# Optimization experiments

Hardware: AMD Instinct MI355X
Metric: run time of the kernel (lower is better)

Reference implementation:

```python
import jax, jax.numpy as jnp
import numpy as np

N, M, C = 32768, 8192, 128
K = 3            # number of interpolation neighbors (PointNet++/RepSurf FP)
EPS_BN = 1e-5    # torch BatchNorm1d default eps
EPS_D = 1e-8     # RepSurf dist_recip eps


def setup_inputs() -> dict:
    key = jax.random.key(0)
    ks = jax.random.split(key, 16)
    s = 0.05
    inp = {
        "pos1": jax.random.normal(ks[0], (N, 3), jnp.float32),
        "pos2": jax.random.normal(ks[1], (M, 3), jnp.float32),
        "feat2": jax.random.normal(ks[2], (M, C), jnp.float32),
    }
    # MLP stack [128,128,128]: Linear + BatchNorm1d (gamma/beta) per layer
    for i in range(3):
        inp[f"W{i}"] = jax.random.normal(ks[3 + i], (C, C), jnp.float32) * s
        inp[f"b{i}"] = jnp.zeros((C,), jnp.float32)
        inp[f"g{i}"] = jnp.ones((C,), jnp.float32)
        inp[f"be{i}"] = jnp.zeros((C,), jnp.float32)
    return inp


def _lin_bn_relu(x, W, b, g, be):
    # Linear -> BatchNorm1d (training-mode batch stats, biased var) -> ReLU
    y = x @ W.T + b
    m = y.mean(axis=0)
    v = y.var(axis=0)
    return jax.nn.relu((y - m) * jax.lax.rsqrt(v + EPS_BN) * g + be)


def reference(pos1, pos2, feat2, W0, b0, g0, be0, W1, b1, g1, be1, W2, b2, g2, be2):
    # squared pairwise distances [N, M] (memory-bound: 1 GB fp32)
    d = ((pos1 ** 2).sum(-1, keepdims=True)
         + (pos2 ** 2).sum(-1)[None, :]
         - 2.0 * (pos1 @ pos2.T))
    neg_d, idx = jax.lax.top_k(-d, K)          # 3 nearest neighbors
    dk = jnp.maximum(-neg_d, 0.0)              # [N, K] squared dists
    w = 1.0 / (dk + EPS_D)
    w = w / w.sum(-1, keepdims=True)           # inverse-distance weights
    # gather neighbor features and interpolate: [N, K, C] -> [N, C]
    interp = jnp.einsum('nkc,nk->nc', feat2[idx], w)
    x = _lin_bn_relu(interp, W0, b0, g0, be0)
    x = _lin_bn_relu(x, W1, b1, g1, be1)
    x = _lin_bn_relu(x, W2, b2, g2, be2)
    return x
```

## Files before the change

### kernel.cpp

```cpp
#include <hip/hip_runtime.h>
#include <hip/hip_fp16.h>
#include <math.h>

#define NQ 32768
#define MC 8192
#define CC 128
#define EPS_BN 1e-5f
#define EPS_D  1e-8

#define DBL_BIG 1e300
#define IDX_BIG 0x7fffffff

#define QB  64
#define TB  256
#define PCE 2048
#define NT  32
#define KM7 0xFFFFFF80u
#define KMASK 0xFFFFE000u
#define IMASK 0x1FFFu
#define NSURV 48
#define KNN_B ((NQ / QB) * 4)
#define GEMM_B (NQ / 64)
#define NGRP 8

typedef __attribute__((ext_vector_type(8))) short bf16x8;
typedef __attribute__((ext_vector_type(8))) _Float16 half8;
typedef __attribute__((ext_vector_type(4))) float floatx4;
typedef __attribute__((ext_vector_type(16))) float floatx16;
typedef unsigned short ushort_t;

__device__ __forceinline__ unsigned bf16pair(float a, float b) {
    unsigned ua = __float_as_uint(a); ua = (ua + 0x7FFFu + ((ua >> 16) & 1u)) >> 16;
    unsigned ub = __float_as_uint(b); ub = (ub + 0x7FFFu + ((ub >> 16) & 1u)) >> 16;
    return ua | (ub << 16);
}
__device__ __forceinline__ ushort_t bf16one(float a) {
    unsigned ua = __float_as_uint(a);
    return (ushort_t)((ua + 0x7FFFu + ((ua >> 16) & 1u)) >> 16);
}
__device__ __forceinline__ float bflo(unsigned u) { return __uint_as_float(u << 16); }
__device__ __forceinline__ float bfhi(unsigned u) { return __uint_as_float(u & 0xFFFF0000u); }

__device__ __forceinline__ void ins3(float& k0, float& k1, float& k2, float x) {
    const float n0 = fminf(k0, x);
    const float n1 = __builtin_amdgcn_fmed3f(k0, k1, x);
    const float n2 = __builtin_amdgcn_fmed3f(k1, k2, x);
    k0 = n0; k1 = n1; k2 = n2;
}

__device__ __forceinline__ unsigned vandor(unsigned d, unsigned m, unsigned ir) {
    unsigned r;
    asm("v_and_or_b32 %0, %1, %2, %3" : "=v"(r) : "v"(d), "s"(m), "v"(ir));
    return r;
}

#define PK2(a, b) ((unsigned)__half_as_ushort(a) | ((unsigned)__half_as_ushort(b) << 16))

__global__ __launch_bounds__(TB) void pack_kernel(const float* __restrict__ pos2,
                                                  uint4* __restrict__ ptile,
                                                  float4* __restrict__ pos2f4) {
    const int c = blockIdx.x * TB + threadIdx.x;
    const float x = pos2[c * 3 + 0];
    const float y = pos2[c * 3 + 1];
    const float z = pos2[c * 3 + 2];
    float4 p4; p4.x = x; p4.y = y; p4.z = z; p4.w = 0.f;
    pos2f4[c] = p4;
    const __half chx = __float2half(x); const float fchx = __half2float(chx);
    const __half chy = __float2half(y); const float fchy = __half2float(chy);
    const __half chz = __float2half(z); const float fchz = __half2float(chz);
    const __half clx = __float2half(x - fchx);
    const __half cly = __float2half(y - fchy);
    const __half clz = __float2half(z - fchz);
    const double X = (double)fchx + (double)__half2float(clx);
    const double Y = (double)fchy + (double)__half2float(cly);
    const double Z = (double)fchz + (double)__half2float(clz);
    const double hc = 0.5 * (X * X + Y * Y + Z * Z);
// ... 94 lines not shown
    float c0 = KINIT, c1 = KINIT, c2 = KINIT;
    float e0 = KINIT, e1 = KINIT, e2 = KINIT;
    unsigned i0 = 0u, i1 = 1u, i2 = 2u, i3 = 3u;
    const unsigned km7 = KM7;
    const floatx16 zc = {0.f,0.f,0.f,0.f,0.f,0.f,0.f,0.f,0.f,0.f,0.f,0.f,0.f,0.f,0.f,0.f};

#define KEY1(v, ir, K0, K1, K2) { \
        const unsigned u_ = vandor(__float_as_uint(v), km7, ir); \
        ins3(K0, K1, K2, __uint_as_float(u_)); }
#define KEYS(d) { \
        KEY1(d[0],  i0, a0, a1, a2); KEY1(d[1],  i1, a0, a1, a2); \
        KEY1(d[2],  i2, a0, a1, a2); KEY1(d[3],  i3, a0, a1, a2); \
        KEY1(d[4],  i0, b0, b1, b2); KEY1(d[5],  i1, b0, b1, b2); \
        KEY1(d[6],  i2, b0, b1, b2); KEY1(d[7],  i3, b0, b1, b2); \
        KEY1(d[8],  i0, c0, c1, c2); KEY1(d[9],  i1, c0, c1, c2); \
        KEY1(d[10], i2, c0, c1, c2); KEY1(d[11], i3, c0, c1, c2); \
        KEY1(d[12], i0, e0, e1, e2); KEY1(d[13], i1, e0, e1, e2); \
        KEY1(d[14], i2, e0, e1, e2); KEY1(d[15], i3, e0, e1, e2); \
        i0 += 4u; i1 += 4u; i2 += 4u; i3 += 4u; }

    uint4 LA = LD(0);
    uint4 LB = LD(1);
    for (int t = 0; t < NT; t += 2) {
        const floatx16 dv = __builtin_amdgcn_mfma_f32_32x32x16_f16(*(const half8*)&LA, bqh, zc, 0, 0, 0);
        LA = LD(t + 2);
        KEYS(dv);
        const floatx16 dw = __builtin_amdgcn_mfma_f32_32x32x16_f16(*(const half8*)&LB, bqh, zc, 0, 0, 0);
        LB = LD(t + 3);
        KEYS(dw);
    }
#undef LD
#undef KEYS
#undef KEY1

#define REKEY(kf, q) __uint_as_float((__float_as_uint(kf) & KMASK) | \
        (unsigned)(cw + (int)((__float_as_uint(kf) & 0x7Fu) >> 2) * 32 + \
                   (int)(__float_as_uint(kf) & 3u) + 8 * (q) + 4 * h))
    float m0 = KINIT, m1 = KINIT, m2 = KINIT;
    ins3(m0, m1, m2, REKEY(a0, 0)); ins3(m0, m1, m2, REKEY(a1, 0)); ins3(m0, m1, m2, REKEY(a2, 0));
    ins3(m0, m1, m2, REKEY(b0, 1)); ins3(m0, m1, m2, REKEY(b1, 1)); ins3(m0, m1, m2, REKEY(b2, 1));
    ins3(m0, m1, m2, REKEY(c0, 2)); ins3(m0, m1, m2, REKEY(c1, 2)); ins3(m0, m1, m2, REKEY(c2, 2));
    ins3(m0, m1, m2, REKEY(e0, 3)); ins3(m0, m1, m2, REKEY(e1, 3)); ins3(m0, m1, m2, REKEY(e2, 3));
#undef REKEY

    {
        const int q = bq * QB + qt * 32 + col;
        unsigned* dst = skeys + (size_t)q * NSURV + piece * 12 + wh * 6 + h * 3;
        dst[0] = __float_as_uint(m0);
        dst[1] = __float_as_uint(m1);
        dst[2] = __float_as_uint(m2);
    }
}

template <int MODE>
__global__ __launch_bounds__(256) void gemm_mfma(const void* __restrict__ Xsrc_,
                                                 const unsigned* __restrict__ skeys,
                                                 const float* __restrict__ pos1,
                                                 const float4* __restrict__ pos2f4,
                                                 const float* __restrict__ statsIn,
                                                 const float* __restrict__ gIn,
                                                 const float* __restrict__ beIn,
                                                 const ushort_t* __restrict__ Wb,
                                                 const float* __restrict__ bias,
                                                 ushort_t* __restrict__ Y,
                                                 float* __restrict__ statsOut) {
    __shared__ __align__(16) short xa[64][136];
    __shared__ __align__(16) short wb[128][136];
    __shared__ float blk_s[CC], blk_q[CC];
    __shared__ float sc_l[CC], sh_l[CC];

    const int row0 = blockIdx.x * 64;

    if constexpr (MODE == 0) {
        const float* feat2 = (const float*)Xsrc_;
        __shared__ int   lidx[QB][3];
        __shared__ float lw[QB][3];
        {
            double* rrd = (double*)&xa[0][0];
            int*    rri = (int*)&wb[0][0];
            const int ql = threadIdx.x >> 2;
            const int pp = threadIdx.x & 3;
            const int qg = row0 + ql;
            const double qx = (double)pos1[qg * 3 + 0];
            const double qy = (double)pos1[qg * 3 + 1];
            const double qz = (double)pos1[qg * 3 + 2];
            double b0 = DBL_BIG, b1 = DBL_BIG, b2 = DBL_BIG;
            int    j0 = IDX_BIG, j1 = IDX_BIG, j2 = IDX_BIG;
            const uint4* kp = (const uint4*)(skeys + (size_t)qg * NSURV + pp * 12);
#pragma unroll
            for (int gi = 0; gi < 3; ++gi) {
                const uint4 kk = kp[gi];
                const unsigned ks[4] = {kk.x, kk.y, kk.z, kk.w};
#pragma unroll
                for (int u = 0; u < 4; ++u) {
                    const int id = (int)(ks[u] & IMASK);
                    const float4 cf = pos2f4[id];
                    const double x = (double)cf.x;
                    const double y = (double)cf.y;
                    const double z = (double)cf.z;
                    const double ax = qx - x, ay = qy - y, az = qz - z;
                    const double d = ax * ax + ay * ay + az * az;
                    const bool l2 = (d < b2) || (d == b2 && id < j2);
                    if (l2) {
                        const bool l1 = (d < b1) || (d == b1 && id < j1);
                        const bool l0 = (d < b0) || (d == b0 && id < j0);
                        b2 = l1 ? b1 : d;              j2 = l1 ? j1 : id;
                        b1 = l1 ? (l0 ? b0 : d) : b1;  j1 = l1 ? (l0 ? j0 : id) : j1;
                        b0 = l0 ? d : b0;              j0 = l0 ? id : j0;
                    }
                }
            }
            const int base = (ql * 4 + pp) * 3;
            rrd[base + 0] = b0; rri[base + 0] = j0;
            rrd[base + 1] = b1; rri[base + 1] = j1;
            rrd[base + 2] = b2; rri[base + 2] = j2;
            __syncthreads();
            if (threadIdx.x < QB) {
                const int qq = threadIdx.x;
                double c0 = DBL_BIG, c1 = DBL_BIG, c2 = DBL_BIG;
                int    i0 = IDX_BIG, i1 = IDX_BIG, i2 = IDX_BIG;
#pragma unroll
                for (int s = 0; s < 12; ++s) {
                    const double d = rrd[qq * 12 + s];
                    const int   id = rri[qq * 12 + s];
                    const bool l2 = (d < c2) || (d == c2 && id < i2);
                    if (l2) {
                        const bool l1 = (d < c1) || (d == c1 && id < i1);
                        const bool l0 = (d < c0) || (d == c0 && id < i0);
                        c2 = l1 ? c1 : d;              i2 = l1 ? i1 : id;
                        c1 = l1 ? (l0 ? c0 : d) : c1;  i1 = l1 ? (l0 ? i0 : id) : i1;
                        c0 = l0 ? d : c0;              i0 = l0 ? id : i0;
                    }
                }
                const double r0 = 1.0 / (c0 + EPS_D);
                const double r1 = 1.0 / (c1 + EPS_D);
                const double r2 = 1.0 / (c2 + EPS_D);
                const double inv = 1.0 / (r0 + r1 + r2);
                lidx[qq][0] = i0; lidx[qq][1] = i1; lidx[qq][2] = i2;
                lw[qq][0] = (float)(r0 * inv);
                lw[qq][1] = (float)(r1 * inv);
                lw[qq][2] = (float)(r2 * inv);
            }
            __syncthreads();
        }
        if (threadIdx.x < CC) { blk_s[threadIdx.x] = 0.f; blk_q[threadIdx.x] = 0.f; }
#pragma unroll
        for (int e = threadIdx.x; e < 64 * 32; e += 256) {
            const int r = e >> 5, c4 = e & 31;
            const int i0 = lidx[r][0], i1 = lidx[r][1], i2 = lidx[r][2];
            const float w0 = lw[r][0], w1 = lw[r][1], w2 = lw[r][2];
            const float4 f0 = *(const float4*)&feat2[(size_t)i0 * CC + c4 * 4];
            const float4 f1 = *(const float4*)&feat2[(size_t)i1 * CC + c4 * 4];
            const float4 f2 = *(const float4*)&feat2[(size_t)i2 * CC + c4 * 4];
            float4 v;
            v.x = w0 * f0.x + w1 * f1.x + w2 * f2.x;
            v.y = w0 * f0.y + w1 * f1.y + w2 * f2.y;
            v.z = w0 * f0.z + w1 * f1.z + w2 * f2.z;
            v.w = w0 * f0.w + w1 * f1.w + w2 * f2.w;
            unsigned* dst = (unsigned*)&xa[r][0];
            dst[c4 * 2 + 0] = bf16pair(v.x, v.y);
            dst[c4 * 2 + 1] = bf16pair(v.z, v.w);
        }
    } else {
        const ushort_t* Xbf = (const ushort_t*)Xsrc_;
        if (threadIdx.x < CC) {
            const int c = threadIdx.x;
            float s = 0.f, q = 0.f;
#pragma unroll
            for (int gr = 0; gr < NGRP; ++gr) {
                s += statsIn[gr * 256 + c];
                q += statsIn[gr * 256 + CC + c];
            }
            const float m = s * (1.f / (float)NQ);
            const float v = fmaf(-m, m, q * (1.f / (float)NQ));
            const float rstd = rsqrtf(v + EPS_BN);
            const float scl = gIn[c] * rstd;
            sc_l[c] = scl;
            sh_l[c] = fmaf(-m, scl, beIn[c]);
            blk_s[c] = 0.f; blk_q[c] = 0.f;
        }
        __syncthreads();
#pragma unroll
        for (int e = threadIdx.x; e < 64 * 16; e += 256) {
            const int r = e >> 4, c8 = e & 15;
            const uint4 u = *(const uint4*)&Xbf[(size_t)(row0 + r) * CC + c8 * 8];
            const float4 s0 = *(const float4*)&sc_l[c8 * 8];
            const float4 s1 = *(const float4*)&sc_l[c8 * 8 + 4];
            const float4 h0 = *(const float4*)&sh_l[c8 * 8];
            const float4 h1 = *(const float4*)&sh_l[c8 * 8 + 4];
            const float v0 = fmaxf(fmaf(bflo(u.x), s0.x, h0.x), 0.f);
            const float v1 = fmaxf(fmaf(bfhi(u.x), s0.y, h0.y), 0.f);
            const float v2 = fmaxf(fmaf(bflo(u.y), s0.z, h0.z), 0.f);
            const float v3 = fmaxf(fmaf(bfhi(u.y), s0.w, h0.w), 0.f);
            const float v4 = fmaxf(fmaf(bflo(u.z), s1.x, h1.x), 0.f);
            const float v5 = fmaxf(fmaf(bfhi(u.z), s1.y, h1.y), 0.f);
            const float v6 = fmaxf(fmaf(bflo(u.w), s1.z, h1.z), 0.f);
            const float v7 = fmaxf(fmaf(bfhi(u.w), s1.w, h1.w), 0.f);
            uint4 o;
            o.x = bf16pair(v0, v1); o.y = bf16pair(v2, v3);
            o.z = bf16pair(v4, v5); o.w = bf16pair(v6, v7);
            *(uint4*)&xa[r][c8 * 8] = o;
        }
    }
#pragma unroll
    for (int e = threadIdx.x; e < 128 * 16; e += 256) {
        const int co = e >> 4, seg = e & 15;
        *(float4*)&wb[co][seg * 8] = *(const float4*)&Wb[(size_t)co * CC + seg * 8];
    }
    __syncthreads();

    const int lane = threadIdx.x & 63;
    const int wv = threadIdx.x >> 6;
    const int nn = lane & 15;
    const int quad = lane >> 4;

    floatx4 acc[8] = {};

    const short* arow = &xa[wv * 16 + nn][0];
#pragma unroll
    for (int ks = 0; ks < 4; ++ks) {
        const bf16x8 a = *(const bf16x8*)(arow + ks * 32 + quad * 8);
#pragma unroll
        for (int ct = 0; ct < 8; ++ct) {
            const bf16x8 b = *(const bf16x8*)(&wb[ct * 16 + nn][0] + ks * 32 + quad * 8);
            acc[ct] = __builtin_amdgcn_mfma_f32_16x16x32_bf16(a, b, acc[ct], 0, 0, 0);
        }
    }

#pragma unroll
    for (int ct = 0; ct < 8; ++ct) {
        const float bv = bias[ct * 16 + nn];
        float s = 0.f, qv = 0.f;
#pragma unroll
        for (int r = 0; r < 4; ++r) {
            acc[ct][r] += bv;
            s += acc[ct][r];
            qv = fmaf(acc[ct][r], acc[ct][r], qv);
        }
#pragma unroll
        for (int r = 0; r < 4; ++r)
            Y[(size_t)(row0 + wv * 16 + quad * 4 + r) * CC + ct * 16 + nn] = bf16one(acc[ct][r]);
        s += __shfl_xor(s, 16, 64); s += __shfl_xor(s, 32, 64);
        qv += __shfl_xor(qv, 16, 64); qv += __shfl_xor(qv, 32, 64);
        if (quad == 0) {
            atomicAdd(&blk_s[ct * 16 + nn], s);
            atomicAdd(&blk_q[ct * 16 + nn], qv);
        }
    }
    __syncthreads();
    {
        const int ch = threadIdx.x;
        const float v = (ch < CC) ? blk_s[ch] : blk_q[ch - CC];
        atomicAdd(&statsOut[(blockIdx.x & (NGRP - 1)) * 256 + ch], v);
    }
}

__global__ __launch_bounds__(256) void bn_final(const ushort_t* __restrict__ Y,
                                                const float* __restrict__ statsIn,
                                                const float* __restrict__ g,
                                                const float* __restrict__ be,
                                                float* __restrict__ out) {
    __shared__ float sc_l[CC], sh_l[CC];
    if (threadIdx.x < CC) {
        const int c = threadIdx.x;
        float s = 0.f, q = 0.f;
#pragma unroll
        for (int gr = 0; gr < NGRP; ++gr) {
            s += statsIn[gr * 256 + c];
            q += statsIn[gr * 256 + CC + c];
        }
        const float m = s * (1.f / (float)NQ);
        const float v = fmaf(-m, m, q * (1.f / (float)NQ));
        const float rstd = rsqrtf(v + EPS_BN);
        const float scl = g[c] * rstd;
        sc_l[c] = scl;
        sh_l[c] = fmaf(-m, scl, be[c]);
    }
    __syncthreads();
    const int base = blockIdx.x * 1024 + threadIdx.x;
#pragma unroll
    for (int it = 0; it < 4; ++it) {
        const int i8 = base + it * 256;
        const int c8 = (i8 & 15) * 8;
        const uint4 u = *(const uint4*)&Y[(size_t)i8 * 8];
        const float4 s0 = *(const float4*)&sc_l[c8];
        const float4 s1 = *(const float4*)&sc_l[c8 + 4];
        const float4 h0 = *(const float4*)&sh_l[c8];
        const float4 h1 = *(const float4*)&sh_l[c8 + 4];
        float4 o0, o1;
        o0.x = fmaxf(fmaf(bflo(u.x), s0.x, h0.x), 0.f);
        o0.y = fmaxf(fmaf(bfhi(u.x), s0.y, h0.y), 0.f);
        o0.z = fmaxf(fmaf(bflo(u.y), s0.z, h0.z), 0.f);
        o0.w = fmaxf(fmaf(bfhi(u.y), s0.w, h0.w), 0.f);
        o1.x = fmaxf(fmaf(bflo(u.z), s1.x, h1.x), 0.f);
        o1.y = fmaxf(fmaf(bfhi(u.z), s1.y, h1.y), 0.f);
        o1.z = fmaxf(fmaf(bflo(u.w), s1.z, h1.z), 0.f);
        o1.w = fmaxf(fmaf(bfhi(u.w), s1.w, h1.w), 0.f);
        ((float4*)out)[i8 * 2 + 0] = o0;
        ((float4*)out)[i8 * 2 + 1] = o1;
    }
}

extern "C" void kernel_launch(void* const* d_in, const int* in_sizes, int n_in,
                              void* d_out, int out_size, void* d_ws, size_t ws_size,
                              hipStream_t stream) {
    (void)in_sizes; (void)n_in; (void)out_size; (void)ws_size;

    const float* pos1  = (const float*)d_in[0];
    const float* pos2  = (const float*)d_in[1];
    const float* feat2 = (const float*)d_in[2];
    const float* Wl[3]  = {(const float*)d_in[3], (const float*)d_in[7],  (const float*)d_in[11]};
    const float* bl[3]  = {(const float*)d_in[4], (const float*)d_in[8],  (const float*)d_in[12]};
    const float* gl[3]  = {(const float*)d_in[5], (const float*)d_in[9],  (const float*)d_in[13]};
    const float* bel[3] = {(const float*)d_in[6], (const float*)d_in[10], (const float*)d_in[14]};

    float* ws = (float*)d_ws;
    ushort_t* B0 = (ushort_t*)ws;
    ushort_t* B1 = B0 + (size_t)NQ * CC;
    unsigned* skeys = (unsigned*)(B1 + (size_t)NQ * CC);
    float* stats = (float*)(skeys + (size_t)NQ * NSURV);
    ushort_t* Wbf = (ushort_t*)(stats + 3 * NGRP * 256);
    uint4* ptile = (uint4*)(Wbf + 3 * CC * CC);
    float4* pos2f4 = (float4*)(ptile + (size_t)258 * 64);

    float* st0 = stats + 0 * NGRP * 256;
    float* st1 = stats + 1 * NGRP * 256;
    float* st2 = stats + 2 * NGRP * 256;

    pack_kernel<<<MC / TB, TB, 0, stream>>>(pos2, ptile, pos2f4);
    knn_kernel<<<KNN_B + 16, TB, 0, stream>>>(pos1, ptile, skeys,
                                              Wl[0], Wl[1], Wl[2], Wbf, stats);
    gemm_mfma<0><<<GEMM_B, 256, 0, stream>>>(feat2, skeys, pos1, pos2f4,
                                             nullptr, nullptr, nullptr,
                                             Wbf + 0 * CC * CC, bl[0], B0, st0);
    gemm_mfma<1><<<GEMM_B, 256, 0, stream>>>(B0, nullptr, nullptr, nullptr,
                                             st0, gl[0], bel[0],
                                             Wbf + 1 * CC * CC, bl[1], B1, st1);
    gemm_mfma<1><<<GEMM_B, 256, 0, stream>>>(B1, nullptr, nullptr, nullptr,
                                             st1, gl[1], bel[1],
                                             Wbf + 2 * CC * CC, bl[2], B0, st2);
    bn_final<<<GEMM_B, 256, 0, stream>>>(B0, st2, gl[2], bel[2], (float*)d_out);
}
```

Baseline: 189.4 us.

## Fuse three MLP layers and final BN into one cooperative kernel with grid syncs

Replaces the three per-layer GEMM launches and the final BN launch with a single cooperative kernel. Each 64-row tile stays in shared memory across layers, and grid.sync() separates the batch-norm statistics phases. This removes the bf16 intermediate round trips through global memory and three kernel launches. It needs all 512 blocks resident at once (at least two per CU), and the grid-wide barriers add their own cost; if the cooperative launch fails, the old multi-kernel path runs instead.

```diff
diff --git a/kernel.cpp b/kernel.cpp
--- a/kernel.cpp
+++ b/kernel.cpp
@@ -1,6 +1,9 @@
 #include <hip/hip_runtime.h>
 #include <hip/hip_fp16.h>
+#include <hip/hip_cooperative_groups.h>
 #include <math.h>
+
+namespace cg = cooperative_groups;
 
 #define NQ 32768
 #define MC 8192
@@ -222,6 +225,271 @@
     }
 }
 
+
+__device__ __forceinline__ void rerank_interp_stage(
+    const float* __restrict__ feat2, const unsigned* __restrict__ skeys,
+    const float* __restrict__ pos1, const float4* __restrict__ pos2f4,
+    int row0, short (*xa)[136], short (*wb)[136],
+    int (*lidx)[3], float (*lw)[3], float* blk_s, float* blk_q)
+{
+    {
+        double* rrd = (double*)&xa[0][0];
+        int*    rri = (int*)&wb[0][0];
+        const int ql = threadIdx.x >> 2;
+        const int pp = threadIdx.x & 3;
+        const int qg = row0 + ql;
+        const double qx = (double)pos1[qg * 3 + 0];
+        const double qy = (double)pos1[qg * 3 + 1];
+        const double qz = (double)pos1[qg * 3 + 2];
+        double b0 = DBL_BIG, b1 = DBL_BIG, b2 = DBL_BIG;
+        int    j0 = IDX_BIG, j1 = IDX_BIG, j2 = IDX_BIG;
+        const uint4* kp = (const uint4*)(skeys + (size_t)qg * NSURV + pp * 12);
+#pragma unroll
+        for (int gi = 0; gi < 3; ++gi) {
+            const uint4 kk = kp[gi];
+            const unsigned ks[4] = {kk.x, kk.y, kk.z, kk.w};
+#pragma unroll
+            for (int u = 0; u < 4; ++u) {
+                const int id = (int)(ks[u] & IMASK);
+                const float4 cf = pos2f4[id];
+                const double x = (double)cf.x;
+                const double y = (double)cf.y;
+                const double z = (double)cf.z;
+                const double ax = qx - x, ay = qy - y, az = qz - z;
+                const double d = ax * ax + ay * ay + az * az;
+                const bool l2 = (d < b2) || (d == b2 && id < j2);
+                if (l2) {
+                    const bool l1 = (d < b1) || (d == b1 && id < j1);
+                    const bool l0 = (d < b0) || (d == b0 && id < j0);
+                    b2 = l1 ? b1 : d;              j2 = l1 ? j1 : id;
+                    b1 = l1 ? (l0 ? b0 : d) : b1;  j1 = l1 ? (l0 ? j0 : id) : j1;
+                    b0 = l0 ? d : b0;              j0 = l0 ? id : j0;
+                }
+            }
+        }
+        const int base = (ql * 4 + pp) * 3;
+        rrd[base + 0] = b0; rri[base + 0] = j0;
+        rrd[base + 1] = b1; rri[base + 1] = j1;
+        rrd[base + 2] = b2; rri[base + 2] = j2;
+        __syncthreads();
+        if (threadIdx.x < QB) {
+            const int qq = threadIdx.x;
+            double c0 = DBL_BIG, c1 = DBL_BIG, c2 = DBL_BIG;
+            int    i0 = IDX_BIG, i1 = IDX_BIG, i2 = IDX_BIG;
+#pragma unroll
+            for (int s = 0; s < 12; ++s) {
+                const double d = rrd[qq * 12 + s];
+                const int   id = rri[qq * 12 + s];
+                const bool l2 = (d < c2) || (d == c2 && id < i2);
+                if (l2) {
+                    const bool l1 = (d < c1) || (d == c1 && id < i1);
+                    const bool l0 = (d < c0) || (d == c0 && id < i0);
+                    c2 = l1 ? c1 : d;              i2 = l1 ? i1 : id;
+                    c1 = l1 ? (l0 ? c0 : d) : c1;  i1 = l1 ? (l0 ? i0 : id) : i1;
+                    c0 = l0 ? d : c0;              i0 = l0 ? id : i0;
+                }
+            }
+            const double r0 = 1.0 / (c0 + EPS_D);
+            const double r1 = 1.0 / (c1 + EPS_D);
+            const double r2 = 1.0 / (c2 + EPS_D);
+            const double inv = 1.0 / (r0 + r1 + r2);
+            lidx[qq][0] = i0; lidx[qq][1] = i1; lidx[qq][2] = i2;
+            lw[qq][0] = (float)(r0 * inv);
+            lw[qq][1] = (float)(r1 * inv);
+            lw[qq][2] = (float)(r2 * inv);
+        }
+        __syncthreads();
+    }
+    if (threadIdx.x < CC) { blk_s[threadIdx.x] = 0.f; blk_q[threadIdx.x] = 0.f; }
+#pragma unroll
+    for (int e = threadIdx.x; e < 64 * 32; e += 256) {
+        const int r = e >> 5, c4 = e & 31;
+        const int i0 = lidx[r][0], i1 = lidx[r][1], i2 = lidx[r][2];
+        const float w0 = lw[r][0], w1 = lw[r][1], w2 = lw[r][2];
+        const float4 f0 = *(const float4*)&feat2[(size_t)i0 * CC + c4 * 4];
+        const float4 f1 = *(const float4*)&feat2[(size_t)i1 * CC + c4 * 4];
+        const float4 f2 = *(const float4*)&feat2[(size_t)i2 * CC + c4 * 4];
+        float4 v;
+        v.x = w0 * f0.x + w1 * f1.x + w2 * f2.x;
+        v.y = w0 * f0.y + w1 * f1.y + w2 * f2.y;
+        v.z = w0 * f0.z + w1 * f1.z + w2 * f2.z;
+        v.w = w0 * f0.w + w1 * f1.w + w2 * f2.w;
+        unsigned* dst = (unsigned*)&xa[r][0];
+        dst[c4 * 2 + 0] = bf16pair(v.x, v.y);
+        dst[c4 * 2 + 1] = bf16pair(v.z, v.w);
+    }
+}
+
+__device__ __forceinline__ void bn_reduce_lds(const float* __restrict__ statsIn,
+                                              const float* __restrict__ g,
+                                              const float* __restrict__ be,
+                                              float* sc_l, float* sh_l,
+                                              float* blk_s, float* blk_q)
+{
+    if (threadIdx.x < CC) {
+        const int c = threadIdx.x;
+        float s = 0.f, q = 0.f;
+#pragma unroll
+        for (int gr = 0; gr < NGRP; ++gr) {
+            s += statsIn[gr * 256 + c];
+            q += statsIn[gr * 256 + CC + c];
+        }
+        const float m = s * (1.f / (float)NQ);
+        const float v = fmaf(-m, m, q * (1.f / (float)NQ));
+        const float rstd = rsqrtf(v + EPS_BN);
+        const float scl = g[c] * rstd;
+        sc_l[c] = scl;
+        sh_l[c] = fmaf(-m, scl, be[c]);
+        blk_s[c] = 0.f; blk_q[c] = 0.f;
+    }
+}
+
+__device__ __forceinline__ void bn_relu_xa(short (*xa)[136],
+                                           const float* sc_l, const float* sh_l)
+{
+#pragma unroll
+    for (int e = threadIdx.x; e < 64 * 16; e += 256) {
+        const int r = e >> 4, c8 = e & 15;
+        const uint4 u = *(const uint4*)&xa[r][c8 * 8];
+        const float4 s0 = *(const float4*)&sc_l[c8 * 8];
+        const float4 s1 = *(const float4*)&sc_l[c8 * 8 + 4];
+        const float4 h0 = *(const float4*)&sh_l[c8 * 8];
+        const float4 h1 = *(const float4*)&sh_l[c8 * 8 + 4];
+        const float v0 = fmaxf(fmaf(bflo(u.x), s0.x, h0.x), 0.f);
+        const float v1 = fmaxf(fmaf(bfhi(u.x), s0.y, h0.y), 0.f);
+        const float v2 = fmaxf(fmaf(bflo(u.y), s0.z, h0.z), 0.f);
+        const float v3 = fmaxf(fmaf(bfhi(u.y), s0.w, h0.w), 0.f);
+        const float v4 = fmaxf(fmaf(bflo(u.z), s1.x, h1.x), 0.f);
+        const float v5 = fmaxf(fmaf(bfhi(u.z), s1.y, h1.y), 0.f);
+        const float v6 = fmaxf(fmaf(bflo(u.w), s1.z, h1.z), 0.f);
+        const float v7 = fmaxf(fmaf(bfhi(u.w), s1.w, h1.w), 0.f);
+        uint4 o;
+        o.x = bf16pair(v0, v1); o.y = bf16pair(v2, v3);
+        o.z = bf16pair(v4, v5); o.w = bf16pair(v6, v7);
+        *(uint4*)&xa[r][c8 * 8] = o;
+    }
+}
+
+__device__ __forceinline__ void layer_mfma_xa(short (*xa)[136], short (*wb)[136],
+                                              float* blk_s, float* blk_q,
+                                              const ushort_t* __restrict__ Wb,
+                                              const float* __restrict__ bias,
+                                              float* __restrict__ statsOut)
+{
+#pragma unroll
+    for (int e = threadIdx.x; e < 128 * 16; e += 256) {
+        const int co = e >> 4, seg = e & 15;
+        *(float4*)&wb[co][seg * 8] = *(const float4*)&Wb[(size_t)co * CC + seg * 8];
+    }
+    __syncthreads();
+
+    const int lane = threadIdx.x & 63;
+    const int wv = threadIdx.x >> 6;
+    const int nn = lane & 15;
+    const int quad = lane >> 4;
+
+    floatx4 acc[8] = {};
+    const short* arow = &xa[wv * 16 + nn][0];
+#pragma unroll
+    for (int ks = 0; ks < 4; ++ks) {
+        const bf16x8 a = *(const bf16x8*)(arow + ks * 32 + quad * 8);
+#pragma unroll
+        for (int ct = 0; ct < 8; ++ct) {
+            const bf16x8 b = *(const bf16x8*)(&wb[ct * 16 + nn][0] + ks * 32 + quad * 8);
+            acc[ct] = __builtin_amdgcn_mfma_f32_16x16x32_bf16(a, b, acc[ct], 0, 0, 0);
+        }
+    }
+    __syncthreads();
+#pragma unroll
+    for (int ct = 0; ct < 8; ++ct) {
+        const float bv = bias[ct * 16 + nn];
+        float s = 0.f, qv = 0.f;
+#pragma unroll
+        for (int r = 0; r < 4; ++r) {
+            acc[ct][r] += bv;
+            s += acc[ct][r];
+            qv = fmaf(acc[ct][r], acc[ct][r], qv);
+        }
+#pragma unroll
+        for (int r = 0; r < 4; ++r)
+            xa[wv * 16 + quad * 4 + r][ct * 16 + nn] = (short)bf16one(acc[ct][r]);
+        s += __shfl_xor(s, 16, 64); s += __shfl_xor(s, 32, 64);
+        qv += __shfl_xor(qv, 16, 64); qv += __shfl_xor(qv, 32, 64);
+        if (quad == 0) {
+            atomicAdd(&blk_s[ct * 16 + nn], s);
+            atomicAdd(&blk_q[ct * 16 + nn], qv);
+        }
+    }
+    __syncthreads();
+    {
+        const int ch = threadIdx.x;
+        const float v = (ch < CC) ? blk_s[ch] : blk_q[ch - CC];
+        atomicAdd(&statsOut[(blockIdx.x & (NGRP - 1)) * 256 + ch], v);
+    }
+}
+
+__global__ __launch_bounds__(256) void gemm_fused(
+        const float* __restrict__ feat2, const unsigned* __restrict__ skeys,
+        const float* __restrict__ pos1, const float4* __restrict__ pos2f4,
+        const ushort_t* __restrict__ Wbf,
+        const float* __restrict__ b0_, const float* __restrict__ b1_, const float* __restrict__ b2_,
+        const float* __restrict__ g0_, const float* __restrict__ g1_, const float* __restrict__ g2_,
+        const float* __restrict__ be0_, const float* __restrict__ be1_, const float* __restrict__ be2_,
+        float* __restrict__ st0, float* __restrict__ st1, float* __restrict__ st2,
+        float* __restrict__ out)
+{
+    __shared__ __align__(16) short xa[64][136];
+    __shared__ __align__(16) short wb[128][136];
+    __shared__ __align__(16) float blk_s[CC], blk_q[CC];
+    __shared__ __align__(16) float sc_l[CC], sh_l[CC];
+    __shared__ int   lidx[QB][3];
+    __shared__ float lw[QB][3];
+
+    cg::grid_group grid = cg::this_grid();
+    const int row0 = blockIdx.x * 64;
+
+    rerank_interp_stage(feat2, skeys, pos1, pos2f4, row0, xa, wb, lidx, lw, blk_s, blk_q);
+    layer_mfma_xa(xa, wb, blk_s, blk_q, Wbf + 0 * CC * CC, b0_, st0);
+    grid.sync();
+
+    bn_reduce_lds(st0, g0_, be0_, sc_l, sh_l, blk_s, blk_q);
+    __syncthreads();
+    bn_relu_xa(xa, sc_l, sh_l);
+    __syncthreads();
+    layer_mfma_xa(xa, wb, blk_s, blk_q, Wbf + 1 * CC * CC, b1_, st1);
+    grid.sync();
+
+    bn_reduce_lds(st1, g1_, be1_, sc_l, sh_l, blk_s, blk_q);
+    __syncthreads();
+    bn_relu_xa(xa, sc_l, sh_l);
+    __syncthreads();
+    layer_mfma_xa(xa, wb, blk_s, blk_q, Wbf + 2 * CC * CC, b2_, st2);
+    grid.sync();
+
+    bn_reduce_lds(st2, g2_, be2_, sc_l, sh_l, blk_s, blk_q);
+    __syncthreads();
+#pragma unroll
+    for (int e = threadIdx.x; e < 64 * 16; e += 256) {
+        const int r = e >> 4, c8 = e & 15;
+        const uint4 u = *(const uint4*)&xa[r][c8 * 8];
+        const float4 s0 = *(const float4*)&sc_l[c8 * 8];
+        const float4 s1 = *(const float4*)&sc_l[c8 * 8 + 4];
+        const float4 h0 = *(const float4*)&sh_l[c8 * 8];
+        const float4 h1 = *(const float4*)&sh_l[c8 * 8 + 4];
+        float4 o0, o1;
+        o0.x = fmaxf(fmaf(bflo(u.x), s0.x, h0.x), 0.f);
+        o0.y = fmaxf(fmaf(bfhi(u.x), s0.y, h0.y), 0.f);
+        o0.z = fmaxf(fmaf(bflo(u.y), s0.z, h0.z), 0.f);
+        o0.w = fmaxf(fmaf(bfhi(u.y), s0.w, h0.w), 0.f);
+        o1.x = fmaxf(fmaf(bflo(u.z), s1.x, h1.x), 0.f);
+        o1.y = fmaxf(fmaf(bfhi(u.z), s1.y, h1.y), 0.f);
+        o1.z = fmaxf(fmaf(bflo(u.w), s1.z, h1.z), 0.f);
+        o1.w = fmaxf(fmaf(bfhi(u.w), s1.w, h1.w), 0.f);
+        float4* op = (float4*)&out[(size_t)(row0 + r) * CC + c8 * 8];
+        op[0] = o0; op[1] = o1;
+    }
+}
+
 template <int MODE>
 __global__ __launch_bounds__(256) void gemm_mfma(const void* __restrict__ Xsrc_,
                                                  const unsigned* __restrict__ skeys,
@@ -236,119 +504,19 @@
                                                  float* __restrict__ statsOut) {
     __shared__ __align__(16) short xa[64][136];
     __shared__ __align__(16) short wb[128][136];
-    __shared__ float blk_s[CC], blk_q[CC];
-    __shared__ float sc_l[CC], sh_l[CC];
+    __shared__ __align__(16) float blk_s[CC], blk_q[CC];
+    __shared__ __align__(16) float sc_l[CC], sh_l[CC];
+    __shared__ int   lidx[QB][3];
+    __shared__ float lw[QB][3];
 
     const int row0 = blockIdx.x * 64;
 
     if constexpr (MODE == 0) {
-        const float* feat2 = (const float*)Xsrc_;
-        __shared__ int   lidx[QB][3];
-        __shared__ float lw[QB][3];
-        {
-            double* rrd = (double*)&xa[0][0];
-            int*    rri = (int*)&wb[0][0];
-            const int ql = threadIdx.x >> 2;
-            const int pp = threadIdx.x & 3;
-            const int qg = row0 + ql;
-            const double qx = (double)pos1[qg * 3 + 0];
-            const double qy = (double)pos1[qg * 3 + 1];
-            const double qz = (double)pos1[qg * 3 + 2];
-            double b0 = DBL_BIG, b1 = DBL_BIG, b2 = DBL_BIG;
-            int    j0 = IDX_BIG, j1 = IDX_BIG, j2 = IDX_BIG;
-            const uint4* kp = (const uint4*)(skeys + (size_t)qg * NSURV + pp * 12);
-#pragma unroll
-            for (int gi = 0; gi < 3; ++gi) {
-                const uint4 kk = kp[gi];
-                const unsigned ks[4] = {kk.x, kk.y, kk.z, kk.w};
-#pragma unroll
-                for (int u = 0; u < 4; ++u) {
-                    const int id = (int)(ks[u] & IMASK);
-                    const float4 cf = pos2f4[id];
-                    const double x = (double)cf.x;
-                    const double y = (double)cf.y;
-                    const double z = (double)cf.z;
-                    const double ax = qx - x, ay = qy - y, az = qz - z;
-                    const double d = ax * ax + ay * ay + az * az;
-                    const bool l2 = (d < b2) || (d == b2 && id < j2);
-                    if (l2) {
-                        const bool l1 = (d < b1) || (d == b1 && id < j1);
-                        const bool l0 = (d < b0) || (d == b0 && id < j0);
-                        b2 = l1 ? b1 : d;              j2 = l1 ? j1 : id;
-                        b1 = l1 ? (l0 ? b0 : d) : b1;  j1 = l1 ? (l0 ? j0 : id) : j1;
-                        b0 = l0 ? d : b0;              j0 = l0 ? id : j0;
-                    }
-                }
-            }
-            const int base = (ql * 4 + pp) * 3;
-            rrd[base + 0] = b0; rri[base + 0] = j0;
-            rrd[base + 1] = b1; rri[base + 1] = j1;
-            rrd[base + 2] = b2; rri[base + 2] = j2;
-            __syncthreads();
-            if (threadIdx.x < QB) {
-                const int qq = threadIdx.x;
-                double c0 = DBL_BIG, c1 = DBL_BIG, c2 = DBL_BIG;
-                int    i0 = IDX_BIG, i1 = IDX_BIG, i2 = IDX_BIG;
-#pragma unroll
-                for (int s = 0; s < 12; ++s) {
-                    const double d = rrd[qq * 12 + s];
-                    const int   id = rri[qq * 12 + s];
-                    const bool l2 = (d < c2) || (d == c2 && id < i2);
-                    if (l2) {
-                        const bool l1 = (d < c1) || (d == c1 && id < i1);
-                        const bool l0 = (d < c0) || (d == c0 && id < i0);
-                        c2 = l1 ? c1 : d;              i2 = l1 ? i1 : id;
-                        c1 = l1 ? (l0 ? c0 : d) : c1;  i1 = l1 ? (l0 ? i0 : id) : i1;
-                        c0 = l0 ? d : c0;              i0 = l0 ? id : i0;
-                    }
-                }
-                const double r0 = 1.0 / (c0 + EPS_D);
-                const double r1 = 1.0 / (c1 + EPS_D);
-                const double r2 = 1.0 / (c2 + EPS_D);
-                const double inv = 1.0 / (r0 + r1 + r2);
-                lidx[qq][0] = i0; lidx[qq][1] = i1; lidx[qq][2] = i2;
-                lw[qq][0] = (float)(r0 * inv);
-                lw[qq][1] = (float)(r1 * inv);
-                lw[qq][2] = (float)(r2 * inv);
-            }
-            __syncthreads();
-        }
-        if (threadIdx.x < CC) { blk_s[threadIdx.x] = 0.f; blk_q[threadIdx.x] = 0.f; }
-#pragma unroll
-        for (int e = threadIdx.x; e < 64 * 32; e += 256) {
-            const int r = e >> 5, c4 = e & 31;
-            const int i0 = lidx[r][0], i1 = lidx[r][1], i2 = lidx[r][2];
-            const float w0 = lw[r][0], w1 = lw[r][1], w2 = lw[r][2];
-            const float4 f0 = *(const float4*)&feat2[(size_t)i0 * CC + c4 * 4];
-            const float4 f1 = *(const float4*)&feat2[(size_t)i1 * CC + c4 * 4];
-            const float4 f2 = *(const float4*)&feat2[(size_t)i2 * CC + c4 * 4];
-            float4 v;
-            v.x = w0 * f0.x + w1 * f1.x + w2 * f2.x;
-            v.y = w0 * f0.y + w1 * f1.y + w2 * f2.y;
-            v.z = w0 * f0.z + w1 * f1.z + w2 * f2.z;
-            v.w = w0 * f0.w + w1 * f1.w + w2 * f2.w;
-            unsigned* dst = (unsigned*)&xa[r][0];
-            dst[c4 * 2 + 0] = bf16pair(v.x, v.y);
-            dst[c4 * 2 + 1] = bf16pair(v.z, v.w);
-        }
+        rerank_interp_stage((const float*)Xsrc_, skeys, pos1, pos2f4, row0,
+                            xa, wb, lidx, lw, blk_s, blk_q);
     } else {
         const ushort_t* Xbf = (const ushort_t*)Xsrc_;
-        if (threadIdx.x < CC) {
-            const int c = threadIdx.x;
-            float s = 0.f, q = 0.f;
-#pragma unroll
-            for (int gr = 0; gr < NGRP; ++gr) {
-                s += statsIn[gr * 256 + c];
-                q += statsIn[gr * 256 + CC + c];
-            }
-            const float m = s * (1.f / (float)NQ);
-            const float v = fmaf(-m, m, q * (1.f / (float)NQ));
-            const float rstd = rsqrtf(v + EPS_BN);
-            const float scl = gIn[c] * rstd;
-            sc_l[c] = scl;
-            sh_l[c] = fmaf(-m, scl, beIn[c]);
-            blk_s[c] = 0.f; blk_q[c] = 0.f;
-        }
+        bn_reduce_lds(statsIn, gIn, beIn, sc_l, sh_l, blk_s, blk_q);
         __syncthreads();
 #pragma unroll
         for (int e = threadIdx.x; e < 64 * 16; e += 256) {
@@ -372,56 +540,12 @@
             *(uint4*)&xa[r][c8 * 8] = o;
         }
     }
-#pragma unroll
-    for (int e = threadIdx.x; e < 128 * 16; e += 256) {
-        const int co = e >> 4, seg = e & 15;
-        *(float4*)&wb[co][seg * 8] = *(const float4*)&Wb[(size_t)co * CC + seg * 8];
-    }
-    __syncthreads();
-
-    const int lane = threadIdx.x & 63;
-    const int wv = threadIdx.x >> 6;
-    const int nn = lane & 15;
-    const int quad = lane >> 4;
-
-    floatx4 acc[8] = {};
-
-    const short* arow = &xa[wv * 16 + nn][0];
-#pragma unroll
-    for (int ks = 0; ks < 4; ++ks) {
-        const bf16x8 a = *(const bf16x8*)(arow + ks * 32 + quad * 8);
-#pragma unroll
-        for (int ct = 0; ct < 8; ++ct) {
-            const bf16x8 b = *(const bf16x8*)(&wb[ct * 16 + nn][0] + ks * 32 + quad * 8);
-            acc[ct] = __builtin_amdgcn_mfma_f32_16x16x32_bf16(a, b, acc[ct], 0, 0, 0);
-        }
-    }
-
-#pragma unroll
-    for (int ct = 0; ct < 8; ++ct) {
-        const float bv = bias[ct * 16 + nn];
-        float s = 0.f, qv = 0.f;
-#pragma unroll
-        for (int r = 0; r < 4; ++r) {
-            acc[ct][r] += bv;
-            s += acc[ct][r];
-            qv = fmaf(acc[ct][r], acc[ct][r], qv);
-        }
-#pragma unroll
-        for (int r = 0; r < 4; ++r)
-            Y[(size_t)(row0 + wv * 16 + quad * 4 + r) * CC + ct * 16 + nn] = bf16one(acc[ct][r]);
-        s += __shfl_xor(s, 16, 64); s += __shfl_xor(s, 32, 64);
-        qv += __shfl_xor(qv, 16, 64); qv += __shfl_xor(qv, 32, 64);
-        if (quad == 0) {
-            atomicAdd(&blk_s[ct * 16 + nn], s);
-            atomicAdd(&blk_q[ct * 16 + nn], qv);
-        }
-    }
-    __syncthreads();
-    {
-        const int ch = threadIdx.x;
-        const float v = (ch < CC) ? blk_s[ch] : blk_q[ch - CC];
-        atomicAdd(&statsOut[(blockIdx.x & (NGRP - 1)) * 256 + ch], v);
+    layer_mfma_xa(xa, wb, blk_s, blk_q, Wb, bias, statsOut);
+    __syncthreads();
+#pragma unroll
+    for (int e = threadIdx.x; e < 64 * 16; e += 256) {
+        const int r = e >> 4, c8 = e & 15;
+        *(uint4*)&Y[(size_t)(row0 + r) * CC + c8 * 8] = *(const uint4*)&xa[r][c8 * 8];
     }
 }
 
@@ -430,22 +554,9 @@
                                                 const float* __restrict__ g,
                                                 const float* __restrict__ be,
                                                 float* __restrict__ out) {
-    __shared__ float sc_l[CC], sh_l[CC];
-    if (threadIdx.x < CC) {
-        const int c = threadIdx.x;
-        float s = 0.f, q = 0.f;
-#pragma unroll
-        for (int gr = 0; gr < NGRP; ++gr) {
-            s += statsIn[gr * 256 + c];
-            q += statsIn[gr * 256 + CC + c];
-        }
-        const float m = s * (1.f / (float)NQ);
-        const float v = fmaf(-m, m, q * (1.f / (float)NQ));
-        const float rstd = rsqrtf(v + EPS_BN);
-        const float scl = g[c] * rstd;
-        sc_l[c] = scl;
-        sh_l[c] = fmaf(-m, scl, be[c]);
-    }
+    __shared__ __align__(16) float sc_l[CC], sh_l[CC];
+    __shared__ float dum_s[CC], dum_q[CC];
+    bn_reduce_lds(statsIn, g, be, sc_l, sh_l, dum_s, dum_q);
     __syncthreads();
     const int base = blockIdx.x * 1024 + threadIdx.x;
 #pragma unroll
@@ -496,18 +607,45 @@
     float* st0 = stats + 0 * NGRP * 256;
     float* st1 = stats + 1 * NGRP * 256;
     float* st2 = stats + 2 * NGRP * 256;
+    float* outp = (float*)d_out;
 
     pack_kernel<<<MC / TB, TB, 0, stream>>>(pos2, ptile, pos2f4);
     knn_kernel<<<KNN_B + 16, TB, 0, stream>>>(pos1, ptile, skeys,
                                               Wl[0], Wl[1], Wl[2], Wbf, stats);
-    gemm_mfma<0><<<GEMM_B, 256, 0, stream>>>(feat2, skeys, pos1, pos2f4,
-                                             nullptr, nullptr, nullptr,
-                                             Wbf + 0 * CC * CC, bl[0], B0, st0);
-    gemm_mfma<1><<<GEMM_B, 256, 0, stream>>>(B0, nullptr, nullptr, nullptr,
-                                             st0, gl[0], bel[0],
-                                             Wbf + 1 * CC * CC, bl[1], B1, st1);
-    gemm_mfma<1><<<GEMM_B, 256, 0, stream>>>(B1, nullptr, nullptr, nullptr,
-                                             st1, gl[1], bel[1],
-                                             Wbf + 2 * CC * CC, bl[2], B0, st2);
-    bn_final<<<GEMM_B, 256, 0, stream>>>(B0, st2, gl[2], bel[2], (float*)d_out);
-}
+
+    static int coop_ok = -1;
+    if (coop_ok < 0) {
+        int nb = 0;
+        hipError_t e = hipOccupancyMaxActiveBlocksPerMultiprocessor(&nb, gemm_fused, 256, 0);
+        coop_ok = (e == hipSuccess && nb >= 2) ? 1 : 0;
+    }
+    bool launched = false;
+    if (coop_ok == 1) {
+        void* f2 = (void*)feat2;  void* sk = (void*)skeys;
+        void* p1 = (void*)pos1;   void* p2 = (void*)pos2f4;
+        void* wb_ = (void*)Wbf;
+        void* a_b0 = (void*)bl[0];  void* a_b1 = (void*)bl[1];  void* a_b2 = (void*)bl[2];
+        void* a_g0 = (void*)gl[0];  void* a_g1 = (void*)gl[1];  void* a_g2 = (void*)gl[2];
+        void* a_e0 = (void*)bel[0]; void* a_e1 = (void*)bel[1]; void* a_e2 = (void*)bel[2];
+        void* a_s0 = (void*)st0;    void* a_s1 = (void*)st1;    void* a_s2 = (void*)st2;
+        void* a_o  = (void*)outp;
+        void* args[] = {&f2, &sk, &p1, &p2, &wb_,
+                        &a_b0, &a_b1, &a_b2, &a_g0, &a_g1, &a_g2,
+                        &a_e0, &a_e1, &a_e2, &a_s0, &a_s1, &a_s2, &a_o};
+        hipError_t e = hipLaunchCooperativeKernel((void*)gemm_fused, dim3(GEMM_B), dim3(256),
+                                                  args, 0, stream);
+        if (e == hipSuccess) launched = true; else coop_ok = 0;
+    }
+    if (!launched) {
+        gemm_mfma<0><<<GEMM_B, 256, 0, stream>>>(feat2, skeys, pos1, pos2f4,
+                                                 nullptr, nullptr, nullptr,
+                                                 Wbf + 0 * CC * CC, bl[0], B0, st0);
+        gemm_mfma<1><<<GEMM_B, 256, 0, stream>>>(B0, nullptr, nullptr, nullptr,
+                                                 st0, gl[0], bel[0],
+                                                 Wbf + 1 * CC * CC, bl[1], B1, st1);
+        gemm_mfma<1><<<GEMM_B, 256, 0, stream>>>(B1, nullptr, nullptr, nullptr,
+                                                 st1, gl[1], bel[1],
+                                                 Wbf + 2 * CC * CC, bl[2], B0, st2);
+        bn_final<<<GEMM_B, 256, 0, stream>>>(B0, st2, gl[2], bel[2], outp);
+    }
+}
```

Result: no change. 189.7 us (+0.2%).

## Split neighbor refine and interpolation out of first GEMM into separate kernel

Applied to the files above, without the earlier changes.

Moves the exact top-3 refinement and inverse-distance feature interpolation out of the first MFMA GEMM into a dedicated kernel with 16 queries per 128-thread block and 8 threads per query. The interpolated features go to global memory as bf16, and the first GEMM then reads them like the later layers, with identity scale and no ReLU. The aim is more parallelism and occupancy for the latency-bound gather and refine phase, which previously ran with 4 threads per query inside a 64-row GEMM block. The cost is one extra launch plus a round trip of an 8 MB bf16 buffer through global memory.

```diff
diff --git a/kernel.cpp b/kernel.cpp
--- a/kernel.cpp
+++ b/kernel.cpp
@@ -22,6 +22,10 @@
 #define KNN_B ((NQ / QB) * 4)
 #define GEMM_B (NQ / 64)
 #define NGRP 8
+
+#define IQ  16
+#define ITB 128
+#define INTERP_B (NQ / IQ)
 
 typedef __attribute__((ext_vector_type(8))) short bf16x8;
 typedef __attribute__((ext_vector_type(8))) _Float16 half8;
@@ -222,11 +226,101 @@
     }
 }
 
+__global__ __launch_bounds__(ITB) void interp_kernel(
+        const float* __restrict__ feat2, const unsigned* __restrict__ skeys,
+        const float* __restrict__ pos1, const float4* __restrict__ pos2f4,
+        ushort_t* __restrict__ Xout) {
+    __shared__ double rrd[IQ * 8 * 3];
+    __shared__ int    rri[IQ * 8 * 3];
+    __shared__ int    lidx[IQ][3];
+    __shared__ float  lw[IQ][3];
+
+    const int row0 = blockIdx.x * IQ;
+    const int ql = threadIdx.x >> 3;
+    const int pp = threadIdx.x & 7;
+    const int qg = row0 + ql;
+
+    {
+        const double qx = (double)pos1[qg * 3 + 0];
+        const double qy = (double)pos1[qg * 3 + 1];
+        const double qz = (double)pos1[qg * 3 + 2];
+        double b0 = DBL_BIG, b1 = DBL_BIG, b2 = DBL_BIG;
+        int    j0 = IDX_BIG, j1 = IDX_BIG, j2 = IDX_BIG;
+        const uint2* kp = (const uint2*)(skeys + (size_t)qg * NSURV + pp * 6);
+        const uint2 ka = kp[0], kb = kp[1], kc = kp[2];
+        const unsigned ks[6] = {ka.x, ka.y, kb.x, kb.y, kc.x, kc.y};
+#pragma unroll
+        for (int u = 0; u < 6; ++u) {
+            const int id = (int)(ks[u] & IMASK);
+            const float4 cf = pos2f4[id];
+            const double x = (double)cf.x;
+            const double y = (double)cf.y;
+            const double z = (double)cf.z;
+            const double ax = qx - x, ay = qy - y, az = qz - z;
+            const double d = ax * ax + ay * ay + az * az;
+            const bool l2 = (d < b2) || (d == b2 && id < j2);
+            if (l2) {
+                const bool l1 = (d < b1) || (d == b1 && id < j1);
+                const bool l0 = (d < b0) || (d == b0 && id < j0);
+                b2 = l1 ? b1 : d;              j2 = l1 ? j1 : id;
+                b1 = l1 ? (l0 ? b0 : d) : b1;  j1 = l1 ? (l0 ? j0 : id) : j1;
+                b0 = l0 ? d : b0;              j0 = l0 ? id : j0;
+            }
+        }
+        const int base = (ql * 8 + pp) * 3;
+        rrd[base + 0] = b0; rri[base + 0] = j0;
+        rrd[base + 1] = b1; rri[base + 1] = j1;
+        rrd[base + 2] = b2; rri[base + 2] = j2;
+        __syncthreads();
+        if (threadIdx.x < IQ) {
+            const int qq = threadIdx.x;
+            double c0 = DBL_BIG, c1 = DBL_BIG, c2 = DBL_BIG;
+            int    i0 = IDX_BIG, i1 = IDX_BIG, i2 = IDX_BIG;
+#pragma unroll
+            for (int s = 0; s < 24; ++s) {
+                const double d = rrd[qq * 24 + s];
+                const int   id = rri[qq * 24 + s];
+                const bool l2 = (d < c2) || (d == c2 && id < i2);
+                if (l2) {
+                    const bool l1 = (d < c1) || (d == c1 && id < i1);
+                    const bool l0 = (d < c0) || (d == c0 && id < i0);
+                    c2 = l1 ? c1 : d;              i2 = l1 ? i1 : id;
+                    c1 = l1 ? (l0 ? c0 : d) : c1;  i1 = l1 ? (l0 ? i0 : id) : i1;
+                    c0 = l0 ? d : c0;              i0 = l0 ? id : i0;
+                }
+            }
+            const double r0 = 1.0 / (c0 + EPS_D);
+            const double r1 = 1.0 / (c1 + EPS_D);
+            const double r2 = 1.0 / (c2 + EPS_D);
+            const double inv = 1.0 / (r0 + r1 + r2);
+            lidx[qq][0] = i0; lidx[qq][1] = i1; lidx[qq][2] = i2;
+            lw[qq][0] = (float)(r0 * inv);
+            lw[qq][1] = (float)(r1 * inv);
+            lw[qq][2] = (float)(r2 * inv);
+        }
+        __syncthreads();
+    }
+#pragma unroll
+    for (int e = threadIdx.x; e < IQ * 32; e += ITB) {
+        const int r = e >> 5, c4 = e & 31;
+        const int i0 = lidx[r][0], i1 = lidx[r][1], i2 = lidx[r][2];
+        const float w0 = lw[r][0], w1 = lw[r][1], w2 = lw[r][2];
+        const float4 f0 = *(const float4*)&feat2[(size_t)i0 * CC + c4 * 4];
+        const float4 f1 = *(const float4*)&feat2[(size_t)i1 * CC + c4 * 4];
+        const float4 f2 = *(const float4*)&feat2[(size_t)i2 * CC + c4 * 4];
+        float4 v;
+        v.x = w0 * f0.x + w1 * f1.x + w2 * f2.x;
+        v.y = w0 * f0.y + w1 * f1.y + w2 * f2.y;
+        v.z = w0 * f0.z + w1 * f1.z + w2 * f2.z;
+        v.w = w0 * f0.w + w1 * f1.w + w2 * f2.w;
+        unsigned* dst = (unsigned*)&Xout[(size_t)(row0 + r) * CC];
+        dst[c4 * 2 + 0] = bf16pair(v.x, v.y);
+        dst[c4 * 2 + 1] = bf16pair(v.z, v.w);
+    }
+}
+
 template <int MODE>
-__global__ __launch_bounds__(256) void gemm_mfma(const void* __restrict__ Xsrc_,
-                                                 const unsigned* __restrict__ skeys,
-                                                 const float* __restrict__ pos1,
-                                                 const float4* __restrict__ pos2f4,
+__global__ __launch_bounds__(256) void gemm_mfma(const ushort_t* __restrict__ Xbf,
                                                  const float* __restrict__ statsIn,
                                                  const float* __restrict__ gIn,
                                                  const float* __restrict__ beIn,
@@ -241,100 +335,9 @@
 
     const int row0 = blockIdx.x * 64;
 
-    if constexpr (MODE == 0) {
-        const float* feat2 = (const float*)Xsrc_;
-        __shared__ int   lidx[QB][3];
-        __shared__ float lw[QB][3];
-        {
-            double* rrd = (double*)&xa[0][0];
-            int*    rri = (int*)&wb[0][0];
-            const int ql = threadIdx.x >> 2;
-            const int pp = threadIdx.x & 3;
-            const int qg = row0 + ql;
-            const double qx = (double)pos1[qg * 3 + 0];
-            const double qy = (double)pos1[qg * 3 + 1];
-            const double qz = (double)pos1[qg * 3 + 2];
-            double b0 = DBL_BIG, b1 = DBL_BIG, b2 = DBL_BIG;
-            int    j0 = IDX_BIG, j1 = IDX_BIG, j2 = IDX_BIG;
-            const uint4* kp = (const uint4*)(skeys + (size_t)qg * NSURV + pp * 12);
-#pragma unroll
-            for (int gi = 0; gi < 3; ++gi) {
-                const uint4 kk = kp[gi];
-                const unsigned ks[4] = {kk.x, kk.y, kk.z, kk.w};
-#pragma unroll
-                for (int u = 0; u < 4; ++u) {
-                    const int id = (int)(ks[u] & IMASK);
-                    const float4 cf = pos2f4[id];
-                    const double x = (double)cf.x;
-                    const double y = (double)cf.y;
-                    const double z = (double)cf.z;
-                    const double ax = qx - x, ay = qy - y, az = qz - z;
-                    const double d = ax * ax + ay * ay + az * az;
-                    const bool l2 = (d < b2) || (d == b2 && id < j2);
-                    if (l2) {
-                        const bool l1 = (d < b1) || (d == b1 && id < j1);
-                        const bool l0 = (d < b0) || (d == b0 && id < j0);
-                        b2 = l1 ? b1 : d;              j2 = l1 ? j1 : id;
-                        b1 = l1 ? (l0 ? b0 : d) : b1;  j1 = l1 ? (l0 ? j0 : id) : j1;
-                        b0 = l0 ? d : b0;              j0 = l0 ? id : j0;
-                    }
-                }
-            }
-            const int base = (ql * 4 + pp) * 3;
-            rrd[base + 0] = b0; rri[base + 0] = j0;
-            rrd[base + 1] = b1; rri[base + 1] = j1;
-            rrd[base + 2] = b2; rri[base + 2] = j2;
-            __syncthreads();
-            if (threadIdx.x < QB) {
-                const int qq = threadIdx.x;
-                double c0 = DBL_BIG, c1 = DBL_BIG, c2 = DBL_BIG;
-                int    i0 = IDX_BIG, i1 = IDX_BIG, i2 = IDX_BIG;
-#pragma unroll
-                for (int s = 0; s < 12; ++s) {
-                    const double d = rrd[qq * 12 + s];
-                    const int   id = rri[qq * 12 + s];
-                    const bool l2 = (d < c2) || (d == c2 && id < i2);
-                    if (l2) {
-                        const bool l1 = (d < c1) || (d == c1 && id < i1);
-                        const bool l0 = (d < c0) || (d == c0 && id < i0);
-                        c2 = l1 ? c1 : d;              i2 = l1 ? i1 : id;
-                        c1 = l1 ? (l0 ? c0 : d) : c1;  i1 = l1 ? (l0 ? i0 : id) : i1;
-                        c0 = l0 ? d : c0;              i0 = l0 ? id : i0;
-                    }
-                }
-                const double r0 = 1.0 / (c0 + EPS_D);
-                const double r1 = 1.0 / (c1 + EPS_D);
-                const double r2 = 1.0 / (c2 + EPS_D);
-                const double inv = 1.0 / (r0 + r1 + r2);
-                lidx[qq][0] = i0; lidx[qq][1] = i1; lidx[qq][2] = i2;
-                lw[qq][0] = (float)(r0 * inv);
-                lw[qq][1] = (float)(r1 * inv);
-                lw[qq][2] = (float)(r2 * inv);
-            }
-            __syncthreads();
-        }
-        if (threadIdx.x < CC) { blk_s[threadIdx.x] = 0.f; blk_q[threadIdx.x] = 0.f; }
-#pragma unroll
-        for (int e = threadIdx.x; e < 64 * 32; e += 256) {
-            const int r = e >> 5, c4 = e & 31;
-            const int i0 = lidx[r][0], i1 = lidx[r][1], i2 = lidx[r][2];
-            const float w0 = lw[r][0], w1 = lw[r][1], w2 = lw[r][2];
-            const float4 f0 = *(const float4*)&feat2[(size_t)i0 * CC + c4 * 4];
-            const float4 f1 = *(const float4*)&feat2[(size_t)i1 * CC + c4 * 4];
-            const float4 f2 = *(const float4*)&feat2[(size_t)i2 * CC + c4 * 4];
-            float4 v;
-            v.x = w0 * f0.x + w1 * f1.x + w2 * f2.x;
-            v.y = w0 * f0.y + w1 * f1.y + w2 * f2.y;
-            v.z = w0 * f0.z + w1 * f1.z + w2 * f2.z;
-            v.w = w0 * f0.w + w1 * f1.w + w2 * f2.w;
-            unsigned* dst = (unsigned*)&xa[r][0];
-            dst[c4 * 2 + 0] = bf16pair(v.x, v.y);
-            dst[c4 * 2 + 1] = bf16pair(v.z, v.w);
-        }
-    } else {
-        const ushort_t* Xbf = (const ushort_t*)Xsrc_;
-        if (threadIdx.x < CC) {
-            const int c = threadIdx.x;
+    if (threadIdx.x < CC) {
+        const int c = threadIdx.x;
+        if constexpr (MODE == 1) {
             float s = 0.f, q = 0.f;
 #pragma unroll
             for (int gr = 0; gr < NGRP; ++gr) {
@@ -347,30 +350,39 @@
             const float scl = gIn[c] * rstd;
             sc_l[c] = scl;
             sh_l[c] = fmaf(-m, scl, beIn[c]);
-            blk_s[c] = 0.f; blk_q[c] = 0.f;
-        }
-        __syncthreads();
-#pragma unroll
-        for (int e = threadIdx.x; e < 64 * 16; e += 256) {
-            const int r = e >> 4, c8 = e & 15;
-            const uint4 u = *(const uint4*)&Xbf[(size_t)(row0 + r) * CC + c8 * 8];
-            const float4 s0 = *(const float4*)&sc_l[c8 * 8];
-            const float4 s1 = *(const float4*)&sc_l[c8 * 8 + 4];
-            const float4 h0 = *(const float4*)&sh_l[c8 * 8];
-            const float4 h1 = *(const float4*)&sh_l[c8 * 8 + 4];
-            const float v0 = fmaxf(fmaf(bflo(u.x), s0.x, h0.x), 0.f);
-            const float v1 = fmaxf(fmaf(bfhi(u.x), s0.y, h0.y), 0.f);
-            const float v2 = fmaxf(fmaf(bflo(u.y), s0.z, h0.z), 0.f);
-            const float v3 = fmaxf(fmaf(bfhi(u.y), s0.w, h0.w), 0.f);
-            const float v4 = fmaxf(fmaf(bflo(u.z), s1.x, h1.x), 0.f);
-            const float v5 = fmaxf(fmaf(bfhi(u.z), s1.y, h1.y), 0.f);
-            const float v6 = fmaxf(fmaf(bflo(u.w), s1.z, h1.z), 0.f);
-            const float v7 = fmaxf(fmaf(bfhi(u.w), s1.w, h1.w), 0.f);
-            uint4 o;
-            o.x = bf16pair(v0, v1); o.y = bf16pair(v2, v3);
-            o.z = bf16pair(v4, v5); o.w = bf16pair(v6, v7);
-            *(uint4*)&xa[r][c8 * 8] = o;
-        }
+        } else {
+            sc_l[c] = 1.f;
+            sh_l[c] = 0.f;
+        }
+        blk_s[c] = 0.f; blk_q[c] = 0.f;
+    }
+    __syncthreads();
+#pragma unroll
+    for (int e = threadIdx.x; e < 64 * 16; e += 256) {
+        const int r = e >> 4, c8 = e & 15;
+        const uint4 u = *(const uint4*)&Xbf[(size_t)(row0 + r) * CC + c8 * 8];
+        const float4 s0 = *(const float4*)&sc_l[c8 * 8];
+        const float4 s1 = *(const float4*)&sc_l[c8 * 8 + 4];
+        const float4 h0 = *(const float4*)&sh_l[c8 * 8];
+        const float4 h1 = *(const float4*)&sh_l[c8 * 8 + 4];
+        float v0 = fmaf(bflo(u.x), s0.x, h0.x);
+        float v1 = fmaf(bfhi(u.x), s0.y, h0.y);
+        float v2 = fmaf(bflo(u.y), s0.z, h0.z);
+        float v3 = fmaf(bfhi(u.y), s0.w, h0.w);
+        float v4 = fmaf(bflo(u.z), s1.x, h1.x);
+        float v5 = fmaf(bfhi(u.z), s1.y, h1.y);
+        float v6 = fmaf(bflo(u.w), s1.z, h1.z);
+        float v7 = fmaf(bfhi(u.w), s1.w, h1.w);
+        if constexpr (MODE == 1) {
+            v0 = fmaxf(v0, 0.f); v1 = fmaxf(v1, 0.f);
+            v2 = fmaxf(v2, 0.f); v3 = fmaxf(v3, 0.f);
+            v4 = fmaxf(v4, 0.f); v5 = fmaxf(v5, 0.f);
+            v6 = fmaxf(v6, 0.f); v7 = fmaxf(v7, 0.f);
+        }
+        uint4 o;
+        o.x = bf16pair(v0, v1); o.y = bf16pair(v2, v3);
+        o.z = bf16pair(v4, v5); o.w = bf16pair(v6, v7);
+        *(uint4*)&xa[r][c8 * 8] = o;
     }
 #pragma unroll
     for (int e = threadIdx.x; e < 128 * 16; e += 256) {
@@ -496,18 +508,17 @@
     float* st0 = stats + 0 * NGRP * 256;
     float* st1 = stats + 1 * NGRP * 256;
     float* st2 = stats + 2 * NGRP * 256;
+    float* outp = (float*)d_out;
 
     pack_kernel<<<MC / TB, TB, 0, stream>>>(pos2, ptile, pos2f4);
     knn_kernel<<<KNN_B + 16, TB, 0, stream>>>(pos1, ptile, skeys,
                                               Wl[0], Wl[1], Wl[2], Wbf, stats);
-    gemm_mfma<0><<<GEMM_B, 256, 0, stream>>>(feat2, skeys, pos1, pos2f4,
-                                             nullptr, nullptr, nullptr,
-                                             Wbf + 0 * CC * CC, bl[0], B0, st0);
-    gemm_mfma<1><<<GEMM_B, 256, 0, stream>>>(B0, nullptr, nullptr, nullptr,
-                                             st0, gl[0], bel[0],
-                                             Wbf + 1 * CC * CC, bl[1], B1, st1);
-    gemm_mfma<1><<<GEMM_B, 256, 0, stream>>>(B1, nullptr, nullptr, nullptr,
-                                             st1, gl[1], bel[1],
-                                             Wbf + 2 * CC * CC, bl[2], B0, st2);
-    bn_final<<<GEMM_B, 256, 0, stream>>>(B0, st2, gl[2], bel[2], (float*)d_out);
-}
+    interp_kernel<<<INTERP_B, ITB, 0, stream>>>(feat2, skeys, pos1, pos2f4, B0);
+    gemm_mfma<2><<<GEMM_B, 256, 0, stream>>>(B0, nullptr, nullptr, nullptr,
+                                             Wbf + 0 * CC * CC, bl[0], B1, st0);
+    gemm_mfma<1><<<GEMM_B, 256, 0, stream>>>(B1, st0, gl[0], bel[0],
+                                             Wbf + 1 * CC * CC, bl[1], B0, st1);
+    gemm_mfma<1><<<GEMM_B, 256, 0, stream>>>(B0, st1, gl[1], bel[1],
+                                             Wbf + 2 * CC * CC, bl[2], B1, st2);
+    bn_final<<<GEMM_B, 256, 0, stream>>>(B1, st2, gl[2], bel[2], outp);
+}
```

New measurement: 192.9 us. About the same (+1.9%).
